# Kernel tuning notes

Hardware: AMD Instinct MI355X
Metric: run time of the kernel (lower is better)

## Reference

```python
import jax, jax.numpy as jnp
import numpy as np

DT = 1e-3
MAX_UPDATE = 0.1


def setup_inputs() -> dict:
    key = jax.random.key(0)
    k1, k2 = jax.random.split(key)
    B, T = 512, 8192
    inputs = jax.random.normal(k1, (B, T, 2), dtype=jnp.float32)
    # learned 2x2 kernel, keras 'uniform' init ~ U(-0.05, 0.05)
    A = jax.random.uniform(k2, (2, 2), dtype=jnp.float32, minval=-0.05, maxval=0.05)
    # physical model coefficients (from coeffs tuple)
    C = jnp.eye(2, dtype=jnp.float32)
    D = 1e-3 * jnp.eye(2, dtype=jnp.float32)
    return {"inputs": inputs, "A": A, "C": C, "D": D}


def reference(inputs, A, C, D):
    # inputs: [B, T, 2] measurement increments dy
    B = inputs.shape[0]
    # initial state per GRNNmodel.initial_state: x0=[1,0], cov0=eye(2)
    x0 = jnp.tile(jnp.array([[1.0, 0.0]], dtype=inputs.dtype), (B, 1))      # [B,2]
    cov0 = jnp.tile(jnp.eye(2, dtype=inputs.dtype)[None], (B, 1, 1))        # [B,2,2]

    Ct = C.T
    Dt = D.T

    def step(carry, dy):
        x, cov = carry                                   # [B,2], [B,2,2]
        out = jnp.einsum('ij,bj->bi', C, x) * DT         # output uses pre-update state
        xicov = cov @ Ct + Dt                            # [B,2,2]
        A_minus_xiC = A - xicov @ C                      # [B,2,2]
        dx = jnp.einsum('bij,bj->bi', A_minus_xiC, x) * DT \
             + jnp.einsum('bij,bj->bi', xicov, dy)
        x_new = x + jnp.clip(dx, -MAX_UPDATE, MAX_UPDATE)
        cov_dt = (jnp.einsum('ij,bjk->bik', A, cov)
                  + jnp.einsum('bij,kj->bik', cov, A)    # cov @ A^T
                  + D
                  - xicov @ jnp.swapaxes(xicov, 1, 2))
        cov_new = jnp.clip(cov + cov_dt * DT, -1.0, 1.0)
        return (x_new, cov_new), out

    dys = jnp.swapaxes(inputs, 0, 1)                     # [T,B,2]
    _, outs = jax.lax.scan(step, (x0, cov0), dys)
    return jnp.swapaxes(outs, 0, 1)                      # [B,T,2]
```

## Files before the change

### kernel.cpp

```cpp
#include <hip/hip_runtime.h>


#define DT_C 1e-3f
#define MAXU 0.1f
#define T_LEN 8192
#define T4 (T_LEN / 2)
#define CHUNK 256
#define G_CHUNK (CHUNK / 2)
#define NCHUNK (T_LEN / CHUNK)

typedef float vfloat4 __attribute__((ext_vector_type(4)));

__device__ __forceinline__ float clipf(float v, float lo, float hi) {
    return fminf(fmaxf(v, lo), hi);
}
#define MEDU(x) __builtin_amdgcn_fmed3f((x), -MAXU, MAXU)
#define SB() __builtin_amdgcn_sched_barrier(0)

__global__ __launch_bounds__(256, 1) void grnn_fused(
    const float* __restrict__ inp, const float* __restrict__ Am,
    const float* __restrict__ Cm, const float* __restrict__ Dm,
    float* __restrict__ out)
{
    __shared__ alignas(16) float pb0[CHUNK];
    __shared__ alignas(16) float pb1[CHUNK];
    __shared__ alignas(16) float pb2[CHUNK];
    __shared__ float4 pbufg[CHUNK];
    __shared__ float4 wlds[2][CHUNK * 2];
    const int tid = threadIdx.x;
    const int wv = tid >> 6;

    if (wv == 1) {
        const int lane = tid & 63;
        const float a00 = Am[0], a01 = Am[1], a10 = Am[2], a11 = Am[3];
        const float c00 = Cm[0], c01 = Cm[1], c10 = Cm[2], c11 = Cm[3];
        const float d00 = Dm[0], d01 = Dm[1], d10 = Dm[2], d11 = Dm[3];
        const bool special = (c00 == 1.f) && (c01 == 0.f) && (c10 == 0.f) &&
                             (c11 == 1.f) && (d01 == 0.f) && (d10 == 0.f);
        const float adt00 = a00 * DT_C, adt01 = a01 * DT_C;
        const float adt10 = a10 * DT_C, adt11 = a11 * DT_C;

        if (special) {
            const float K00 = 1.f + 2.f * adt00, A2dt01 = 2.f * adt01;
            const float K11 = 1.f + 2.f * adt11, A2dt10 = 2.f * adt10;
            const float K01 = 1.f + (a00 + a11) * DT_C;
            const float cd0 = DT_C * d00, cd1 = DT_C * d11;
            float p00 = 1.f, p01 = 0.f, p11 = 1.f;

#define PSTEP(Q0, Q1, Q2, F)                                                  \
            {                                                                 \
                Q0.F = p00; Q1.F = p01; Q2.F = p11;                           \
                const float xi00 = p00 + d00;                                 \
                const float xi11 = p11 + d11;                                 \
                const float s2  = p01 * p01;                                  \
                const float q00 = fmaf(xi00, xi00, s2);                       \
                const float q11 = fmaf(xi11, xi11, s2);                       \
                const float q01 = p01 * (xi00 + xi11);                        \
                const float t00 = fmaf(K00, p00, fmaf(A2dt01, p01, cd0));     \
                const float t11 = fmaf(A2dt10, p01, fmaf(K11, p11, cd1));     \
                const float t01 = fmaf(adt10, p00,                            \
                                       fmaf(K01, p01, adt01 * p11));          \
                p00 = fmaf(-DT_C, q00, t00);                                  \
                p01 = fmaf(-DT_C, q01, t01);                                  \
                p11 = fmaf(-DT_C, q11, t11);                                  \
            }

#define PBLOCK8(QA0, QA1, QA2, QB0, QB1, QB2, I)                              \
            {                                                                 \
                PSTEP(QA0, QA1, QA2, x) PSTEP(QA0, QA1, QA2, y)               \
                PSTEP(QA0, QA1, QA2, z) PSTEP(QA0, QA1, QA2, w)               \
                PSTEP(QB0, QB1, QB2, x) PSTEP(QB0, QB1, QB2, y)               \
                PSTEP(QB0, QB1, QB2, z) PSTEP(QB0, QB1, QB2, w)               \
                *(vfloat4*)&pb0[(I)]     = QA0;                               \
                *(vfloat4*)&pb0[(I) + 4] = QB0;                               \
                *(vfloat4*)&pb1[(I)]     = QA1;                               \
                *(vfloat4*)&pb1[(I) + 4] = QB1;                               \
                *(vfloat4*)&pb2[(I)]     = QA2;                               \
                *(vfloat4*)&pb2[(I) + 4] = QB2;                               \
            }

            for (int it = 0; it <= NCHUNK; ++it) {
                if (it < NCHUNK) {
                    if (lane == 0) {
                        for (int i = 0; i < CHUNK; i += 16) {
                            vfloat4 qa0, qa1, qa2, qb0, qb1, qb2;
                            vfloat4 qc0, qc1, qc2, qd0, qd1, qd2;
                            PBLOCK8(qa0, qa1, qa2, qb0, qb1, qb2, i)
                            PBLOCK8(qc0, qc1, qc2, qd0, qd1, qd2, i + 8)
                            asm volatile("" ::
                                "v"(qa0), "v"(qa1), "v"(qa2),
                                "v"(qb0), "v"(qb1), "v"(qb2));
                        }
                    }
                    __builtin_amdgcn_wave_barrier();
                    float4* dst = wlds[it & 1];
#pragma unroll
                    for (int k = 0; k < 4; ++k) {
                        const int i = k * 64 + lane;
                        const float pv0 = pb0[i], pv1 = pb1[i], pv2 = pb2[i];
                        const float xi00 = pv0 + d00, xi01 = pv1, xi11 = pv2 + d11;
                        float4 mv, xv;
                        mv.x = fmaf(-DT_C, xi00, adt00);
                        mv.y = fmaf(-DT_C, xi01, adt10);
                        mv.z = fmaf(-DT_C, xi01, adt01);
                        mv.w = fmaf(-DT_C, xi11, adt11);
                        xv = make_float4(xi00, xi01, xi01, xi11);
                        dst[2 * i]     = mv;
                        dst[2 * i + 1] = xv;
                    }
                }
                __syncthreads();
            }
#undef PBLOCK8
#undef PSTEP
        } else {
            float p00 = 1.f, p01 = 0.f, p10 = 0.f, p11 = 1.f;
            for (int it = 0; it <= NCHUNK; ++it) {
                if (it < NCHUNK) {
                    if (lane == 0) {
                        for (int i = 0; i < CHUNK; ++i) {
                            pbufg[i] = make_float4(p00, p01, p10, p11);
                            const float xi00 = p00*c00 + p01*c01 + d00;
                            const float xi01 = p00*c10 + p01*c11 + d10;
                            const float xi10 = p10*c00 + p11*c01 + d01;
                            const float xi11 = p10*c10 + p11*c11 + d11;
                            const float g00 = a00*p00 + a01*p10 + p00*a00 + p01*a01 + d00 - (xi00*xi00 + xi01*xi01);
                            const float g01 = a00*p01 + a01*p11 + p00*a10 + p01*a11 + d01 - (xi00*xi10 + xi01*xi11);
                            const float g10 = a10*p00 + a11*p10 + p10*a00 + p11*a01 + d10 - (xi10*xi00 + xi11*xi01);
                            const float g11 = a10*p01 + a11*p11 + p10*a10 + p11*a11 + d11 - (xi10*xi10 + xi11*xi11);
                            p00 = clipf(p00 + g00 * DT_C, -1.f, 1.f);
                            p01 = clipf(p01 + g01 * DT_C, -1.f, 1.f);
                            p10 = clipf(p10 + g10 * DT_C, -1.f, 1.f);
                            p11 = clipf(p11 + g11 * DT_C, -1.f, 1.f);
                        }
                    }
                    __builtin_amdgcn_wave_barrier();
                    float4* dst = wlds[it & 1];
#pragma unroll
                    for (int k = 0; k < 4; ++k) {
                        const int i = k * 64 + lane;
                        const float4 pv = pbufg[i];
                        const float xi00 = pv.x*c00 + pv.y*c01 + d00;
                        const float xi01 = pv.x*c10 + pv.y*c11 + d10;
                        const float xi10 = pv.z*c00 + pv.w*c01 + d01;
                        const float xi11 = pv.z*c10 + pv.w*c11 + d11;
                        const float m00 = a00 - (xi00*c00 + xi01*c10);
                        const float m01 = a01 - (xi00*c01 + xi01*c11);
                        const float m10 = a10 - (xi10*c00 + xi11*c10);
                        const float m11 = a11 - (xi10*c01 + xi11*c11);
                        float4 mv, xv;
                        mv.x = m00 * DT_C; mv.y = m10 * DT_C;
                        mv.z = m01 * DT_C; mv.w = m11 * DT_C;
                        xv = make_float4(xi00, xi10, xi01, xi11);
                        dst[2 * i]     = mv;
                        dst[2 * i + 1] = xv;
                    }
                }
                __syncthreads();
            }
        }
    } else if (wv == 0) {
        const int lane = tid;
        const int b = blockIdx.x * 64 + lane;
        const float cdt00 = Cm[0] * DT_C, cdt01 = Cm[1] * DT_C;
        const float cdt10 = Cm[2] * DT_C, cdt11 = Cm[3] * DT_C;
        const float4* __restrict__ in4 =
            reinterpret_cast<const float4*>(inp) + (size_t)b * T4;
        float4* __restrict__ out4 =
            reinterpret_cast<float4*>(out) + (size_t)b * T4;

        float x0 = 1.f, x1 = 0.f;
        float4 d0 = in4[0], d1 = in4[1], d2 = in4[2], d3 = in4[3];
        float4 d4 = in4[4], d5 = in4[5], d6 = in4[6], d7 = in4[7];
        float4 s0a, s0b, s0c, s0d, s1a, s1b, s1c, s1d;
        float4 t0a, t0b, t0c, t0d, t1a, t1b, t1c, t1d;

#define WLG(P, G)                                                             \
        { P##a = wbuf[4*(G)];   P##b = wbuf[4*(G)+1];                         \
          P##c = wbuf[4*(G)+2]; P##d = wbuf[4*(G)+3]; }

#define GRANC(P, DJ, OG)                                                      \
        {                                                                     \
            const float4 dyv = DJ;                                            \
            const int nog = (OG) + 8;                                         \
            DJ = in4[nog < T4 ? nog : (T4 - 1)];                              \
            float4 ov;                                                        \
            ov.x = fmaf(cdt00, x0, cdt01 * x1);                               \
            ov.y = fmaf(cdt10, x0, cdt11 * x1);                               \
            float e0 = fmaf(P##b.x, dyv.x, P##b.z * dyv.y);                   \
            float e1 = fmaf(P##b.y, dyv.x, P##b.w * dyv.y);                   \
            float dx0 = fmaf(P##a.x, x0, fmaf(P##a.z, x1, e0));               \
            float dx1 = fmaf(P##a.y, x0, fmaf(P##a.w, x1, e1));               \
            x0 += MEDU(dx0);                                                  \
            x1 += MEDU(dx1);                                                  \
            ov.z = fmaf(cdt00, x0, cdt01 * x1);                               \
            ov.w = fmaf(cdt10, x0, cdt11 * x1);                               \
            e0 = fmaf(P##d.x, dyv.z, P##d.z * dyv.w);                         \
            e1 = fmaf(P##d.y, dyv.z, P##d.w * dyv.w);                         \
            dx0 = fmaf(P##c.x, x0, fmaf(P##c.z, x1, e0));                     \
            dx1 = fmaf(P##c.y, x0, fmaf(P##c.w, x1, e1));                     \
            x0 += MEDU(dx0);                                                  \
            x1 += MEDU(dx1);                                                  \
            out4[OG] = ov;                                                    \
        }

        for (int it = 0; it <= NCHUNK; ++it) {
            if (it > 0) {
                const int cc = it - 1;
                const float4* wbuf = wlds[cc & 1];
                const int ogc = cc * G_CHUNK;
                WLG(s0, 0) WLG(s1, 1)
                SB();
                for (int q = 0; q < G_CHUNK / 8; ++q) {
                    const int g = 8 * q;
                    const int og = ogc + g;
                    WLG(t0, g + 2) WLG(t1, g + 3)
                    SB();
                    GRANC(s0, d0, og)     GRANC(s1, d1, og + 1)
                    SB();
                    WLG(s0, g + 4) WLG(s1, g + 5)
                    SB();
                    GRANC(t0, d2, og + 2) GRANC(t1, d3, og + 3)
                    SB();
                    WLG(t0, g + 6) WLG(t1, g + 7)
                    SB();
                    GRANC(s0, d4, og + 4) GRANC(s1, d5, og + 5)
                    SB();
                    {
                        const int gn0 = (g + 8 < G_CHUNK) ? (g + 8) : (G_CHUNK - 1);
                        const int gn1 = (g + 9 < G_CHUNK) ? (g + 9) : (G_CHUNK - 1);
                        WLG(s0, gn0) WLG(s1, gn1)
                    }
                    SB();
                    GRANC(t0, d6, og + 6) GRANC(t1, d7, og + 7)
                    SB();
                }
            }
            __syncthreads();
        }
#undef GRANC
#undef WLG
    } else {
        for (int it = 0; it <= NCHUNK; ++it) __syncthreads();
    }
}

__global__ __launch_bounds__(64) void grnn_mono(
    const float* __restrict__ inp, const float* __restrict__ Am,
    const float* __restrict__ Cm, const float* __restrict__ Dm,
    float* __restrict__ out, int B)
{
    const int b = blockIdx.x * blockDim.x + threadIdx.x;
    if (b >= B) return;
    const float a00 = Am[0], a01 = Am[1], a10 = Am[2], a11 = Am[3];
    const float c00 = Cm[0], c01 = Cm[1], c10 = Cm[2], c11 = Cm[3];
    const float d00 = Dm[0], d01 = Dm[1], d10 = Dm[2], d11 = Dm[3];
    float x0 = 1.0f, x1 = 0.0f;
    float p00 = 1.0f, p01 = 0.0f, p10 = 0.0f, p11 = 1.0f;
    const float2* __restrict__ in2 = reinterpret_cast<const float2*>(inp) + (size_t)b * T_LEN;
    float2* __restrict__ out2 = reinterpret_cast<float2*>(out) + (size_t)b * T_LEN;
#pragma unroll 4
    for (int t = 0; t < T_LEN; ++t) {
        float2 o;
        o.x = (c00 * x0 + c01 * x1) * DT_C;
        o.y = (c10 * x0 + c11 * x1) * DT_C;
        out2[t] = o;
        const float xi00 = p00 * c00 + p01 * c01 + d00;
        const float xi01 = p00 * c10 + p01 * c11 + d10;
        const float xi10 = p10 * c00 + p11 * c01 + d01;
        const float xi11 = p10 * c10 + p11 * c11 + d11;
        const float m00 = a00 - (xi00 * c00 + xi01 * c10);
        const float m01 = a01 - (xi00 * c01 + xi01 * c11);
        const float m10 = a10 - (xi10 * c00 + xi11 * c10);
        const float m11 = a11 - (xi10 * c01 + xi11 * c11);
        const float2 dy = in2[t];
        float dx0 = (m00 * x0 + m01 * x1) * DT_C + xi00 * dy.x + xi01 * dy.y;
        float dx1 = (m10 * x0 + m11 * x1) * DT_C + xi10 * dy.x + xi11 * dy.y;
        x0 += clipf(dx0, -MAXU, MAXU);
        x1 += clipf(dx1, -MAXU, MAXU);
        const float g00 = a00*p00 + a01*p10 + p00*a00 + p01*a01 + d00 - (xi00*xi00 + xi01*xi01);
        const float g01 = a00*p01 + a01*p11 + p00*a10 + p01*a11 + d01 - (xi00*xi10 + xi01*xi11);
        const float g10 = a10*p00 + a11*p10 + p10*a00 + p11*a01 + d10 - (xi10*xi00 + xi11*xi01);
        const float g11 = a10*p01 + a11*p11 + p10*a10 + p11*a11 + d11 - (xi10*xi10 + xi11*xi11);
        p00 = clipf(p00 + g00 * DT_C, -1.0f, 1.0f);
        p01 = clipf(p01 + g01 * DT_C, -1.0f, 1.0f);
        p10 = clipf(p10 + g10 * DT_C, -1.0f, 1.0f);
        p11 = clipf(p11 + g11 * DT_C, -1.0f, 1.0f);
    }
}

extern "C" void kernel_launch(void* const* d_in, const int* in_sizes, int n_in,
                              void* d_out, int out_size, void* d_ws, size_t ws_size,
                              hipStream_t stream) {
    const float* inp = (const float*)d_in[0];
    const float* Am  = (const float*)d_in[1];
    const float* Cm  = (const float*)d_in[2];
    const float* Dm  = (const float*)d_in[3];
    float* out = (float*)d_out;
    const int B = in_sizes[0] / (T_LEN * 2);

    if ((B % 64) == 0) {
        hipLaunchKernelGGL(grnn_fused, dim3(B / 64), dim3(256), 0, stream,
                           inp, Am, Cm, Dm, out);
    } else {
        hipLaunchKernelGGL(grnn_mono, dim3((B + 63) / 64), dim3(64), 0, stream,
                           inp, Am, Cm, Dm, out, B);
    }
}
```

Measured before the change: 497.3 us.

## Transpose input/output to time-major layout around the recurrent scan kernel

Adds a tiled float4 transpose kernel that rearranges inputs into a time-major workspace, so each step of the scan reads and writes a contiguous 1 KB line across the 64 batch lanes instead of strided per-row accesses. A copy of the fused kernel operates on the transposed buffers, and a second transpose restores the batch-major output. This trades two extra full-tensor passes through HBM for coalesced memory access in the latency-bound sequential loop. It depends on a large workspace and B==512.

```diff
diff --git a/kernel.cpp b/kernel.cpp
--- a/kernel.cpp
+++ b/kernel.cpp
@@ -8,6 +8,7 @@
 #define CHUNK 256
 #define G_CHUNK (CHUNK / 2)
 #define NCHUNK (T_LEN / CHUNK)
+#define BROWS 512
 
 typedef float vfloat4 __attribute__((ext_vector_type(4)));
 
@@ -17,10 +18,28 @@
 #define MEDU(x) __builtin_amdgcn_fmed3f((x), -MAXU, MAXU)
 #define SB() __builtin_amdgcn_sched_barrier(0)
 
-__global__ __launch_bounds__(256, 1) void grnn_fused(
-    const float* __restrict__ inp, const float* __restrict__ Am,
+__global__ __launch_bounds__(256) void transpose_f4(
+    const float4* __restrict__ src, float4* __restrict__ dst,
+    int rows, int cols)
+{
+    __shared__ float4 tile[32][33];
+    const int tx = threadIdx.x & 31;
+    const int ty = threadIdx.x >> 5;
+    const int c0 = blockIdx.x * 32;
+    const int r0 = blockIdx.y * 32;
+#pragma unroll
+    for (int i = 0; i < 32; i += 8)
+        tile[ty + i][tx] = src[(size_t)(r0 + ty + i) * cols + (c0 + tx)];
+    __syncthreads();
+#pragma unroll
+    for (int i = 0; i < 32; i += 8)
+        dst[(size_t)(c0 + ty + i) * rows + (r0 + tx)] = tile[tx][ty + i];
+}
+
+__global__ __launch_bounds__(256, 1) void grnn_fused_t(
+    const float4* __restrict__ inT, const float* __restrict__ Am,
     const float* __restrict__ Cm, const float* __restrict__ Dm,
-    float* __restrict__ out)
+    float4* __restrict__ outT)
 {
     __shared__ alignas(16) float pb0[CHUNK];
     __shared__ alignas(16) float pb1[CHUNK];
@@ -164,6 +183,230 @@
         const int b = blockIdx.x * 64 + lane;
         const float cdt00 = Cm[0] * DT_C, cdt01 = Cm[1] * DT_C;
         const float cdt10 = Cm[2] * DT_C, cdt11 = Cm[3] * DT_C;
+
+        float x0 = 1.f, x1 = 0.f;
+        float4 d0 = inT[(size_t)0 * BROWS + b], d1 = inT[(size_t)1 * BROWS + b];
+        float4 d2 = inT[(size_t)2 * BROWS + b], d3 = inT[(size_t)3 * BROWS + b];
+        float4 d4 = inT[(size_t)4 * BROWS + b], d5 = inT[(size_t)5 * BROWS + b];
+        float4 d6 = inT[(size_t)6 * BROWS + b], d7 = inT[(size_t)7 * BROWS + b];
+        float4 s0a, s0b, s0c, s0d, s1a, s1b, s1c, s1d;
+        float4 t0a, t0b, t0c, t0d, t1a, t1b, t1c, t1d;
+
+#define WLG(P, G)                                                             \
+        { P##a = wbuf[4*(G)];   P##b = wbuf[4*(G)+1];                         \
+          P##c = wbuf[4*(G)+2]; P##d = wbuf[4*(G)+3]; }
+
+#define GRANC(P, DJ, OG)                                                      \
+        {                                                                     \
+            const float4 dyv = DJ;                                            \
+            const int nog = (OG) + 8;                                         \
+            const int rg = nog < T4 ? nog : (T4 - 1);      \
+            DJ = inT[(size_t)rg * BROWS + b];                                 \
+            float4 ov;                                                        \
+            ov.x = fmaf(cdt00, x0, cdt01 * x1);                               \
+            ov.y = fmaf(cdt10, x0, cdt11 * x1);                               \
+            float e0 = fmaf(P##b.x, dyv.x, P##b.z * dyv.y);                   \
+            float e1 = fmaf(P##b.y, dyv.x, P##b.w * dyv.y);                   \
+            float dx0 = fmaf(P##a.x, x0, fmaf(P##a.z, x1, e0));               \
+            float dx1 = fmaf(P##a.y, x0, fmaf(P##a.w, x1, e1));               \
+            x0 += MEDU(dx0);                                                  \
+            x1 += MEDU(dx1);                                                  \
+            ov.z = fmaf(cdt00, x0, cdt01 * x1);                               \
+            ov.w = fmaf(cdt10, x0, cdt11 * x1);                               \
+            e0 = fmaf(P##d.x, dyv.z, P##d.z * dyv.w);                         \
+            e1 = fmaf(P##d.y, dyv.z, P##d.w * dyv.w);                         \
+            dx0 = fmaf(P##c.x, x0, fmaf(P##c.z, x1, e0));                     \
+            dx1 = fmaf(P##c.y, x0, fmaf(P##c.w, x1, e1));                     \
+            x0 += MEDU(dx0);                                                  \
+            x1 += MEDU(dx1);                                                  \
+            outT[(size_t)(OG) * BROWS + b] = ov;                              \
+        }
+
+        for (int it = 0; it <= NCHUNK; ++it) {
+            if (it > 0) {
+                const int cc = it - 1;
+                const float4* wbuf = wlds[cc & 1];
+                const int ogc = cc * G_CHUNK;
+                WLG(s0, 0) WLG(s1, 1)
+                SB();
+                for (int q = 0; q < G_CHUNK / 8; ++q) {
+                    const int g = 8 * q;
+                    const int og = ogc + g;
+                    WLG(t0, g + 2) WLG(t1, g + 3)
+                    SB();
+                    GRANC(s0, d0, og)     GRANC(s1, d1, og + 1)
+                    SB();
+                    WLG(s0, g + 4) WLG(s1, g + 5)
+                    SB();
+                    GRANC(t0, d2, og + 2) GRANC(t1, d3, og + 3)
+                    SB();
+                    WLG(t0, g + 6) WLG(t1, g + 7)
+                    SB();
+                    GRANC(s0, d4, og + 4) GRANC(s1, d5, og + 5)
+                    SB();
+                    {
+                        const int gn0 = (g + 8 < G_CHUNK) ? (g + 8) : (G_CHUNK - 1);
+                        const int gn1 = (g + 9 < G_CHUNK) ? (g + 9) : (G_CHUNK - 1);
+                        WLG(s0, gn0) WLG(s1, gn1)
+                    }
+                    SB();
+                    GRANC(t0, d6, og + 6) GRANC(t1, d7, og + 7)
+                    SB();
+                }
+            }
+            __syncthreads();
+        }
+#undef GRANC
+#undef WLG
+    } else {
+        for (int it = 0; it <= NCHUNK; ++it) __syncthreads();
+    }
+}
+
+__global__ __launch_bounds__(256, 1) void grnn_fused(
+    const float* __restrict__ inp, const float* __restrict__ Am,
+    const float* __restrict__ Cm, const float* __restrict__ Dm,
+    float* __restrict__ out)
+{
+    __shared__ alignas(16) float pb0[CHUNK];
+    __shared__ alignas(16) float pb1[CHUNK];
+    __shared__ alignas(16) float pb2[CHUNK];
+    __shared__ float4 pbufg[CHUNK];
+    __shared__ float4 wlds[2][CHUNK * 2];
+    const int tid = threadIdx.x;
+    const int wv = tid >> 6;
+
+    if (wv == 1) {
+        const int lane = tid & 63;
+        const float a00 = Am[0], a01 = Am[1], a10 = Am[2], a11 = Am[3];
+        const float c00 = Cm[0], c01 = Cm[1], c10 = Cm[2], c11 = Cm[3];
+        const float d00 = Dm[0], d01 = Dm[1], d10 = Dm[2], d11 = Dm[3];
+        const bool special = (c00 == 1.f) && (c01 == 0.f) && (c10 == 0.f) &&
+                             (c11 == 1.f) && (d01 == 0.f) && (d10 == 0.f);
+        const float adt00 = a00 * DT_C, adt01 = a01 * DT_C;
+        const float adt10 = a10 * DT_C, adt11 = a11 * DT_C;
+
+        if (special) {
+            const float K00 = 1.f + 2.f * adt00, A2dt01 = 2.f * adt01;
+            const float K11 = 1.f + 2.f * adt11, A2dt10 = 2.f * adt10;
+            const float K01 = 1.f + (a00 + a11) * DT_C;
+            const float cd0 = DT_C * d00, cd1 = DT_C * d11;
+            float p00 = 1.f, p01 = 0.f, p11 = 1.f;
+#define PSTEP(Q0, Q1, Q2, F)                                                  \
+            {                                                                 \
+                Q0.F = p00; Q1.F = p01; Q2.F = p11;                           \
+                const float xi00 = p00 + d00;                                 \
+                const float xi11 = p11 + d11;                                 \
+                const float s2  = p01 * p01;                                  \
+                const float q00 = fmaf(xi00, xi00, s2);                       \
+                const float q11 = fmaf(xi11, xi11, s2);                       \
+                const float q01 = p01 * (xi00 + xi11);                        \
+                const float t00 = fmaf(K00, p00, fmaf(A2dt01, p01, cd0));     \
+                const float t11 = fmaf(A2dt10, p01, fmaf(K11, p11, cd1));     \
+                const float t01 = fmaf(adt10, p00,                            \
+                                       fmaf(K01, p01, adt01 * p11));          \
+                p00 = fmaf(-DT_C, q00, t00);                                  \
+                p01 = fmaf(-DT_C, q01, t01);                                  \
+                p11 = fmaf(-DT_C, q11, t11);                                  \
+            }
+#define PBLOCK8(QA0, QA1, QA2, QB0, QB1, QB2, I)                              \
+            {                                                                 \
+                PSTEP(QA0, QA1, QA2, x) PSTEP(QA0, QA1, QA2, y)               \
+                PSTEP(QA0, QA1, QA2, z) PSTEP(QA0, QA1, QA2, w)               \
+                PSTEP(QB0, QB1, QB2, x) PSTEP(QB0, QB1, QB2, y)               \
+                PSTEP(QB0, QB1, QB2, z) PSTEP(QB0, QB1, QB2, w)               \
+                *(vfloat4*)&pb0[(I)]     = QA0;                               \
+                *(vfloat4*)&pb0[(I) + 4] = QB0;                               \
+                *(vfloat4*)&pb1[(I)]     = QA1;                               \
+                *(vfloat4*)&pb1[(I) + 4] = QB1;                               \
+                *(vfloat4*)&pb2[(I)]     = QA2;                               \
+                *(vfloat4*)&pb2[(I) + 4] = QB2;                               \
+            }
+            for (int it = 0; it <= NCHUNK; ++it) {
+                if (it < NCHUNK) {
+                    if (lane == 0) {
+                        for (int i = 0; i < CHUNK; i += 16) {
+                            vfloat4 qa0, qa1, qa2, qb0, qb1, qb2;
+                            vfloat4 qc0, qc1, qc2, qd0, qd1, qd2;
+                            PBLOCK8(qa0, qa1, qa2, qb0, qb1, qb2, i)
+                            PBLOCK8(qc0, qc1, qc2, qd0, qd1, qd2, i + 8)
+                            asm volatile("" ::
+                                "v"(qa0), "v"(qa1), "v"(qa2),
+                                "v"(qb0), "v"(qb1), "v"(qb2));
+                        }
+                    }
+                    __builtin_amdgcn_wave_barrier();
+                    float4* dst = wlds[it & 1];
+#pragma unroll
+                    for (int k = 0; k < 4; ++k) {
+                        const int i = k * 64 + lane;
+                        const float pv0 = pb0[i], pv1 = pb1[i], pv2 = pb2[i];
+                        const float xi00 = pv0 + d00, xi01 = pv1, xi11 = pv2 + d11;
+                        float4 mv, xv;
+                        mv.x = fmaf(-DT_C, xi00, adt00);
+                        mv.y = fmaf(-DT_C, xi01, adt10);
+                        mv.z = fmaf(-DT_C, xi01, adt01);
+                        mv.w = fmaf(-DT_C, xi11, adt11);
+                        xv = make_float4(xi00, xi01, xi01, xi11);
+                        dst[2 * i]     = mv;
+                        dst[2 * i + 1] = xv;
+                    }
+                }
+                __syncthreads();
+            }
+#undef PBLOCK8
+#undef PSTEP
+        } else {
+            float p00 = 1.f, p01 = 0.f, p10 = 0.f, p11 = 1.f;
+            for (int it = 0; it <= NCHUNK; ++it) {
+                if (it < NCHUNK) {
+                    if (lane == 0) {
+                        for (int i = 0; i < CHUNK; ++i) {
+                            pbufg[i] = make_float4(p00, p01, p10, p11);
+                            const float xi00 = p00*c00 + p01*c01 + d00;
+                            const float xi01 = p00*c10 + p01*c11 + d10;
+                            const float xi10 = p10*c00 + p11*c01 + d01;
+                            const float xi11 = p10*c10 + p11*c11 + d11;
+                            const float g00 = a00*p00 + a01*p10 + p00*a00 + p01*a01 + d00 - (xi00*xi00 + xi01*xi01);
+                            const float g01 = a00*p01 + a01*p11 + p00*a10 + p01*a11 + d01 - (xi00*xi10 + xi01*xi11);
+                            const float g10 = a10*p00 + a11*p10 + p10*a00 + p11*a01 + d10 - (xi10*xi00 + xi11*xi01);
+                            const float g11 = a10*p01 + a11*p11 + p10*a10 + p11*a11 + d11 - (xi10*xi10 + xi11*xi11);
+                            p00 = clipf(p00 + g00 * DT_C, -1.f, 1.f);
+                            p01 = clipf(p01 + g01 * DT_C, -1.f, 1.f);
+                            p10 = clipf(p10 + g10 * DT_C, -1.f, 1.f);
+                            p11 = clipf(p11 + g11 * DT_C, -1.f, 1.f);
+                        }
+                    }
+                    __builtin_amdgcn_wave_barrier();
+                    float4* dst = wlds[it & 1];
+#pragma unroll
+                    for (int k = 0; k < 4; ++k) {
+                        const int i = k * 64 + lane;
+                        const float4 pv = pbufg[i];
+                        const float xi00 = pv.x*c00 + pv.y*c01 + d00;
+                        const float xi01 = pv.x*c10 + pv.y*c11 + d10;
+                        const float xi10 = pv.z*c00 + pv.w*c01 + d01;
+                        const float xi11 = pv.z*c10 + pv.w*c11 + d11;
+                        const float m00 = a00 - (xi00*c00 + xi01*c10);
+                        const float m01 = a01 - (xi00*c01 + xi01*c11);
+                        const float m10 = a10 - (xi10*c00 + xi11*c10);
+                        const float m11 = a11 - (xi10*c01 + xi11*c11);
+                        float4 mv, xv;
+                        mv.x = m00 * DT_C; mv.y = m10 * DT_C;
+                        mv.z = m01 * DT_C; mv.w = m11 * DT_C;
+                        xv = make_float4(xi00, xi10, xi01, xi11);
+                        dst[2 * i]     = mv;
+                        dst[2 * i + 1] = xv;
+                    }
+                }
+                __syncthreads();
+            }
+        }
+    } else if (wv == 0) {
+        const int lane = tid;
+        const int b = blockIdx.x * 64 + lane;
+        const float cdt00 = Cm[0] * DT_C, cdt01 = Cm[1] * DT_C;
+        const float cdt10 = Cm[2] * DT_C, cdt11 = Cm[3] * DT_C;
         const float4* __restrict__ in4 =
             reinterpret_cast<const float4*>(inp) + (size_t)b * T4;
         float4* __restrict__ out4 =
@@ -178,7 +421,6 @@
 #define WLG(P, G)                                                             \
         { P##a = wbuf[4*(G)];   P##b = wbuf[4*(G)+1];                         \
           P##c = wbuf[4*(G)+2]; P##d = wbuf[4*(G)+3]; }
-
 #define GRANC(P, DJ, OG)                                                      \
         {                                                                     \
             const float4 dyv = DJ;                                            \
@@ -299,7 +541,21 @@
     float* out = (float*)d_out;
     const int B = in_sizes[0] / (T_LEN * 2);
 
-    if ((B % 64) == 0) {
+    const size_t need_ws = (size_t)2 * T4 * BROWS * sizeof(float4);
+
+    if (B == BROWS && d_ws != nullptr && ws_size >= need_ws) {
+        float4* inT  = (float4*)d_ws;
+        float4* outT = inT + (size_t)T4 * BROWS;
+        hipLaunchKernelGGL(transpose_f4, dim3(T4 / 32, BROWS / 32), dim3(256),
+                           0, stream,
+                           reinterpret_cast<const float4*>(inp), inT,
+                           BROWS, T4);
+        hipLaunchKernelGGL(grnn_fused_t, dim3(BROWS / 64), dim3(256), 0, stream,
+                           inT, Am, Cm, Dm, outT);
+        hipLaunchKernelGGL(transpose_f4, dim3(BROWS / 32, T4 / 32), dim3(256),
+                           0, stream,
+                           outT, reinterpret_cast<float4*>(out), T4, BROWS);
+    } else if ((B % 64) == 0) {
         hipLaunchKernelGGL(grnn_fused, dim3(B / 64), dim3(256), 0, stream,
                            inp, Am, Cm, Dm, out);
     } else {
```

Measured after the change: 515.0 us. 3.6% more time.
